# Optimization experiments

Measured on AMD Instinct MI355X. Metric: run time of the kernel, lower is better.

## Reference

```python
import jax, jax.numpy as jnp
import numpy as np

B, T, I, H, O = 64, 128, 512, 1024, 512

def setup_inputs() -> dict:
    key = jax.random.key(0)
    ks = jax.random.split(key, 4)
    std = 1.0 / np.sqrt(H)
    xs = jax.random.normal(ks[0], (B, T, I), dtype=jnp.float32)
    # fused gate weights: order (i, f, g, o)
    W_ih = jax.random.uniform(ks[1], (I, 4 * H), minval=-std, maxval=std, dtype=jnp.float32)
    W_hh = jax.random.uniform(ks[2], (H, 4 * H), minval=-std, maxval=std, dtype=jnp.float32)
    b = jnp.zeros((4 * H,), dtype=jnp.float32)
    W_o = jax.random.uniform(ks[3], (H, O), minval=-std, maxval=std, dtype=jnp.float32)
    b_o = jnp.zeros((O,), dtype=jnp.float32)
    return {"xs": xs, "W_ih": W_ih, "W_hh": W_hh, "b": b, "W_o": W_o, "b_o": b_o}

def reference(xs, W_ih, W_hh, b, W_o, b_o):
    act = jax.nn.relu  # activation='relu' replaces tanh in the cell
    # precompute input contribution for all timesteps: [B, T, 4H]
    x_gates = jnp.einsum('bti,ig->btg', xs, W_ih) + b

    def step(carry, xg):
        h, c = carry
        gates = xg + h @ W_hh  # [B, 4H]
        i, f, g, o = jnp.split(gates, 4, axis=-1)
        i = jax.nn.sigmoid(i)
        f = jax.nn.sigmoid(f)
        g = act(g)
        o = jax.nn.sigmoid(o)
        c = f * c + i * g
        h = o * act(c)
        return (h, c), None

    h0 = jnp.zeros((xs.shape[0], W_hh.shape[0]), dtype=xs.dtype)
    c0 = jnp.zeros_like(h0)
    (h_t, _), _ = jax.lax.scan(step, (h0, c0), jnp.swapaxes(x_gates, 0, 1))
    return h_t @ W_o + b_o  # [B, O]
```

## Files before the change

kernel.cpp:

```cpp
#include <hip/hip_runtime.h>

typedef unsigned int uint;
typedef unsigned short ushort;
typedef __attribute__((ext_vector_type(8))) short short8;
typedef __attribute__((ext_vector_type(16))) float f32x16;
typedef __attribute__((ext_vector_type(4))) uint uintx4;

#define T_STEPS 128
#define NGRP 128

__device__ __forceinline__ ushort f2bf(float f) {
  union { float f; uint u; } v; v.f = f;
  uint r = v.u + 0x7fffu + ((v.u >> 16) & 1u);
  return (ushort)(r >> 16);
}
__device__ __forceinline__ float bf2f(ushort u) {
  union { uint u; float f; } v; v.u = ((uint)u) << 16;
  return v.f;
}

union F8 { uint4 u4; short8 s; };
union F8v { uintx4 u; short8 s; };


__global__ void convert_xs_kernel(const float* __restrict__ xs, ushort* __restrict__ xb) {
  int idx = blockIdx.x * 256 + threadIdx.x;
  int t = idx >> 12;
  int b = (idx >> 6) & 63;
  int j = idx & 63;
  const float* src = xs + (b * 128 + t) * 512 + j * 8;
  float4 a = *(const float4*)src;
  float4 c = *(const float4*)(src + 4);
  union { ushort r[8]; uint4 v; } p;
  p.r[0] = f2bf(a.x); p.r[1] = f2bf(a.y); p.r[2] = f2bf(a.z); p.r[3] = f2bf(a.w);
  p.r[4] = f2bf(c.x); p.r[5] = f2bf(c.y); p.r[6] = f2bf(c.z); p.r[7] = f2bf(c.w);
  *(uint4*)(xb + t * 32768 + j * 512 + b * 8) = p.v;
}

__global__ void transpose_w_kernel(const float* __restrict__ W, ushort* __restrict__ WT, int ko) {
  __shared__ ushort tile[32][33];
  int kt = blockIdx.x * 32, nt = blockIdx.y * 32;
  int tx = threadIdx.x & 31, ty = threadIdx.x >> 5;
#pragma unroll
  for (int i = 0; i < 4; ++i) {
    int kk = ty + i * 8;
    tile[kk][tx] = f2bf(W[(kt + kk) * 4096 + nt + tx]);
  }
  __syncthreads();
#pragma unroll
  for (int i = 0; i < 4; ++i) {
    int nn = ty + i * 8;
    WT[(nt + nn) * 1536 + ko + kt + tx] = tile[tx][nn];
  }
}


__global__ __launch_bounds__(512, 1) void lstm_persist(
    const ushort* __restrict__ xsb, const ushort* __restrict__ WT,
    const float* __restrict__ bias, const float* __restrict__ Wo,
    const float* __restrict__ bo, ushort* __restrict__ hbuf,
    uint* __restrict__ flg, float* __restrict__ out) {

  __shared__ float sP[8 * 2 * 16 * 64];

  const int tid = threadIdx.x;
  const int wg  = blockIdx.x;
  const int lane = tid & 63;
  const int wv = tid >> 6;
  const int c  = lane & 31;
  const int hi = lane >> 5;
  const int rep = wg >> 6;
  const int wgu = wg & 63;

  const int gc0 = ((c >> 4)) * 1024 + wgu * 16 + (c & 15);
  const int gc1 = (2 + (c >> 4)) * 1024 + wgu * 16 + (c & 15);
  uint4 Wx[4][2], Wh[8][2];
#pragma unroll
  for (int kf = 0; kf < 4; ++kf) {
    int k = wv * 64 + kf * 16 + hi * 8;
    Wx[kf][0] = *(const uint4*)(WT + gc0 * 1536 + k);
    Wx[kf][1] = *(const uint4*)(WT + gc1 * 1536 + k);
  }
#pragma unroll
  for (int i = 0; i < 8; ++i) {
    int k = 512 + (wv * 8 + i) * 16 + hi * 8;
    Wh[i][0] = *(const uint4*)(WT + gc0 * 1536 + k);
    Wh[i][1] = *(const uint4*)(WT + gc1 * 1536 + k);
  }

  const float bc0 = bias[gc0];
  const float bc1 = bias[gc1];
  const int r0f = wv * 2;
  float cst[2] = {0.f, 0.f};

  for (int t = 0; t < T_STEPS; ++t) {
    const ushort* __restrict__ hrd = hbuf + t * 65536 + rep * 32768;
    ushort* __restrict__ hwr = hbuf + (t + 1) * 65536 + rep * 32768;

    uint4 Ax[4];
    {
      const ushort* xst = xsb + t * 32768 + rep * 256 + c * 8;
#pragma unroll
      for (int kf = 0; kf < 4; ++kf)
        Ax[kf] = *(const uint4*)(xst + (wv * 8 + kf * 2 + hi) * 512);
    }
    f32x16 acc0 = {}, acc1 = {};
#pragma unroll
    for (int kf = 0; kf < 4; ++kf) {
      F8 a, w0, w1; a.u4 = Ax[kf]; w0.u4 = Wx[kf][0]; w1.u4 = Wx[kf][1];
      acc0 = __builtin_amdgcn_mfma_f32_32x32x16_bf16(a.s, w0.s, acc0, 0, 0, 0);
      acc1 = __builtin_amdgcn_mfma_f32_32x32x16_bf16(a.s, w1.s, acc1, 0, 0, 0);
    }

    uintx4 Ah[8];
    {
      const ushort* hb = hrd + (wv * 8) * 512 + c * 16 + hi * 8;
      bool allok;
      do {
#pragma unroll
        for (int i = 0; i < 8; ++i)
          asm volatile("global_load_dwordx4 %0, %1, off sc1"
                       : "=v"(Ah[i]) : "v"(hb + i * 512) : "memory");
        asm volatile("s_waitcnt vmcnt(0)" ::: "memory");
        __builtin_amdgcn_sched_barrier(0);
        bool ok = true;
#pragma unroll
        for (int i = 0; i < 8; ++i)
          ok = ok && ((Ah[i].x & 0xFFFFu) != 0xFFFFu) && ((Ah[i].w >> 16) != 0xFFFFu);
        allok = __all(ok);
        if (!allok) __builtin_amdgcn_s_sleep(1);
      } while (!allok);
    }
#pragma unroll
    for (int i = 0; i < 8; ++i) {
      F8v a; F8 w0, w1; a.u = Ah[i]; w0.u4 = Wh[i][0]; w1.u4 = Wh[i][1];
      acc0 = __builtin_amdgcn_mfma_f32_32x32x16_bf16(a.s, w0.s, acc0, 0, 0, 0);
      acc1 = __builtin_amdgcn_mfma_f32_32x32x16_bf16(a.s, w1.s, acc1, 0, 0, 0);
    }

    {
      float* p = sP + wv * 2048 + lane;
#pragma unroll
      for (int r = 0; r < 16; ++r) p[r * 64] = acc0[r];
#pragma unroll
      for (int r = 0; r < 16; ++r) p[1024 + r * 64] = acc1[r];
    }
    __syncthreads();

#pragma unroll
    for (int s = 0; s < 2; ++s) {
      int r = r0f + s;
      int o = r * 64 + lane;
      float f0 = bc0, f1 = bc1;
#pragma unroll
      for (int w = 0; w < 8; ++w) {
        f0 += sP[w * 2048 + o];
        f1 += sP[w * 2048 + 1024 + o];
      }
      float ff = __shfl_xor(f0, 16);
      float oo = __shfl_xor(f1, 16);
      float ig = 1.f / (1.f + __expf(-f0));
      float fg = 1.f / (1.f + __expf(-ff));
      float gg = fmaxf(f1, 0.f);
      float og = 1.f / (1.f + __expf(-oo));
      float cn = fg * cst[s] + ig * gg;
      cst[s] = cn;
      ushort hv = f2bf(og * fmaxf(cn, 0.f));
      int hvi = (int)(uint)hv;
      uint q0 = ((uint)hvi & 0xFFFFu) | ((uint)__shfl_xor(hvi, 1) << 16);
      uint q1 = (uint)__shfl_xor((int)q0, 2);
      uint q2 = (uint)__shfl_xor((int)q0, 4);
      uint q3 = (uint)__shfl_xor((int)q1, 4);
      if ((lane & 23) == 0) {
        int row = (r & 3) + 8 * (r >> 2) + 4 * hi;
        int half = (lane >> 3) & 1;
        uintx4 g; g.x = q0; g.y = q1; g.z = q2; g.w = q3;
        asm volatile("global_store_dwordx4 %0, %1, off sc1"
                     :: "v"(hwr + wgu * 512 + row * 16 + half * 8), "v"(g) : "memory");
      }
    }
    __syncthreads();
  }

  asm volatile("s_waitcnt vmcnt(0)" ::: "memory");
  __syncthreads();
  if (tid == 0)
    __hip_atomic_store(flg + (rep * 64 + wgu) * 32, 1u,
                       __ATOMIC_RELAXED, __HIP_MEMORY_SCOPE_AGENT);

  if (tid < 64) {
    const uint* fp = flg + (rep * 64 + tid) * 32;
    while (__hip_atomic_load(fp, __ATOMIC_RELAXED, __HIP_MEMORY_SCOPE_AGENT) < 1u)
      __builtin_amdgcn_s_sleep(2);
  }
  __syncthreads();
  if (tid < 256) {
    int oidx = wg * 256 + tid;
    int b = oidx >> 9, oc = oidx & 511;
    int rep2 = b >> 5, row = b & 31;
    const ushort* hf = hbuf + T_STEPS * 65536 + rep2 * 32768 + row * 16;
    float s = bo[oc];
#pragma unroll 2
    for (int w = 0; w < 64; ++w) {
      uint4 h0 = *(const uint4*)(hf + w * 512);
      uint4 h1 = *(const uint4*)(hf + w * 512 + 8);
      const ushort* p0 = (const ushort*)&h0;
      const ushort* p1 = (const ushort*)&h1;
#pragma unroll
      for (int j = 0; j < 8; ++j)
        s = fmaf(bf2f(p0[j]), Wo[(w * 16 + j) * 512 + oc], s);
#pragma unroll
      for (int j = 0; j < 8; ++j)
        s = fmaf(bf2f(p1[j]), Wo[(w * 16 + 8 + j) * 512 + oc], s);
    }
    out[oidx] = s;
  }
}


extern "C" void kernel_launch(void* const* d_in, const int* in_sizes, int n_in,
                              void* d_out, int out_size, void* d_ws, size_t ws_size,
                              hipStream_t stream) {
  (void)in_sizes; (void)n_in; (void)out_size; (void)ws_size;
  const float* xs  = (const float*)d_in[0];
  const float* Wih = (const float*)d_in[1];
  const float* Whh = (const float*)d_in[2];
  const float* b   = (const float*)d_in[3];
  const float* Wo  = (const float*)d_in[4];
  const float* bo  = (const float*)d_in[5];
  float* out = (float*)d_out;

  char* ws = (char*)d_ws;
  uint* flg    = (uint*)ws;
  ushort* hbuf = (ushort*)(ws + 16384);
  ushort* xsb  = (ushort*)(ws + 16384 + 16908288);
  ushort* WT   = (ushort*)(ws + 16384 + 16908288 + 8388608);

  hipMemsetAsync(ws, 0, 16384, stream);
  hipMemsetAsync(hbuf, 0xFF, 16908288, stream);
  hipMemsetAsync(hbuf, 0x00, 131072, stream);
  convert_xs_kernel<<<2048, 256, 0, stream>>>(xs, xsb);
  transpose_w_kernel<<<dim3(16, 128), 256, 0, stream>>>(Wih, WT, 0);
  transpose_w_kernel<<<dim3(32, 128), 256, 0, stream>>>(Whh, WT, 512);
  lstm_persist<<<NGRP, 512, 0, stream>>>(xsb, WT, b, Wo, bo, hbuf, flg, out);
}
```

Measured before the change: 406.8 us.

## Precompute next step's input projection and double-buffer LDS to drop a barrier

Computes the x·W_ih MFMA contribution for step t+1 during step t, after the recurrent h load and the LDS partial write, so this work no longer sits between consecutive h-dependency waits. The shared-memory partial-sum buffer is double-buffered, which lets the trailing __syncthreads per step be removed. This costs extra accumulator registers and doubles LDS use to 128KB. On the last iteration it also does a wasted wrap-around load of step 0.

```diff
diff --git a/kernel.cpp b/kernel.cpp
--- a/kernel.cpp
+++ b/kernel.cpp
@@ -61,7 +61,7 @@
     const float* __restrict__ bo, ushort* __restrict__ hbuf,
     uint* __restrict__ flg, float* __restrict__ out) {
 
-  __shared__ float sP[8 * 2 * 16 * 64];
+  __shared__ float sP[2][8 * 2048];
 
   const int tid = threadIdx.x;
   const int wg  = blockIdx.x;
@@ -93,23 +93,35 @@
   const int r0f = wv * 2;
   float cst[2] = {0.f, 0.f};
 
-  for (int t = 0; t < T_STEPS; ++t) {
-    const ushort* __restrict__ hrd = hbuf + t * 65536 + rep * 32768;
-    ushort* __restrict__ hwr = hbuf + (t + 1) * 65536 + rep * 32768;
-
+  f32x16 acc0 = {}, acc1 = {};
+  {
+    const ushort* xst = xsb + rep * 256 + c * 8;
     uint4 Ax[4];
-    {
-      const ushort* xst = xsb + t * 32768 + rep * 256 + c * 8;
-#pragma unroll
-      for (int kf = 0; kf < 4; ++kf)
-        Ax[kf] = *(const uint4*)(xst + (wv * 8 + kf * 2 + hi) * 512);
-    }
-    f32x16 acc0 = {}, acc1 = {};
+#pragma unroll
+    for (int kf = 0; kf < 4; ++kf)
+      Ax[kf] = *(const uint4*)(xst + (wv * 8 + kf * 2 + hi) * 512);
 #pragma unroll
     for (int kf = 0; kf < 4; ++kf) {
       F8 a, w0, w1; a.u4 = Ax[kf]; w0.u4 = Wx[kf][0]; w1.u4 = Wx[kf][1];
       acc0 = __builtin_amdgcn_mfma_f32_32x32x16_bf16(a.s, w0.s, acc0, 0, 0, 0);
       acc1 = __builtin_amdgcn_mfma_f32_32x32x16_bf16(a.s, w1.s, acc1, 0, 0, 0);
+    }
+  }
+
+  float* sPcur = &sP[0][0];
+  float* sPnxt = &sP[1][0];
+
+  for (int t = 0; t < T_STEPS; ++t) {
+    const ushort* __restrict__ hrd = hbuf + t * 65536 + rep * 32768;
+    ushort* __restrict__ hwr = hbuf + (t + 1) * 65536 + rep * 32768;
+
+    uint4 Ax[4];
+    {
+      const int tn = (t + 1) & 127;
+      const ushort* xst = xsb + tn * 32768 + rep * 256 + c * 8;
+#pragma unroll
+      for (int kf = 0; kf < 4; ++kf)
+        Ax[kf] = *(const uint4*)(xst + (wv * 8 + kf * 2 + hi) * 512);
     }
 
     uintx4 Ah[8];
@@ -139,12 +151,21 @@
     }
 
     {
-      float* p = sP + wv * 2048 + lane;
+      float* p = sPcur + wv * 2048 + lane;
 #pragma unroll
       for (int r = 0; r < 16; ++r) p[r * 64] = acc0[r];
 #pragma unroll
       for (int r = 0; r < 16; ++r) p[1024 + r * 64] = acc1[r];
     }
+
+    f32x16 accN0 = {}, accN1 = {};
+#pragma unroll
+    for (int kf = 0; kf < 4; ++kf) {
+      F8 a, w0, w1; a.u4 = Ax[kf]; w0.u4 = Wx[kf][0]; w1.u4 = Wx[kf][1];
+      accN0 = __builtin_amdgcn_mfma_f32_32x32x16_bf16(a.s, w0.s, accN0, 0, 0, 0);
+      accN1 = __builtin_amdgcn_mfma_f32_32x32x16_bf16(a.s, w1.s, accN1, 0, 0, 0);
+    }
+
     __syncthreads();
 
 #pragma unroll
@@ -154,8 +175,8 @@
       float f0 = bc0, f1 = bc1;
 #pragma unroll
       for (int w = 0; w < 8; ++w) {
-        f0 += sP[w * 2048 + o];
-        f1 += sP[w * 2048 + 1024 + o];
+        f0 += sPcur[w * 2048 + o];
+        f1 += sPcur[w * 2048 + 1024 + o];
       }
       float ff = __shfl_xor(f0, 16);
       float oo = __shfl_xor(f1, 16);
@@ -179,7 +200,9 @@
                      :: "v"(hwr + wgu * 512 + row * 16 + half * 8), "v"(g) : "memory");
       }
     }
-    __syncthreads();
+
+    acc0 = accN0; acc1 = accN1;
+    float* tmp = sPcur; sPcur = sPnxt; sPnxt = tmp;
   }
 
   asm volatile("s_waitcnt vmcnt(0)" ::: "memory");
```

Measured after the change: 562.5 us. 38.3% more time.
